# Kernel optimization log

Hardware: AMD Instinct MI355X
Metric: run time of the kernel (lower is better)

## Reference

```python
import jax, jax.numpy as jnp
import numpy as np

N_NODES = 50000
NUM_FEATS = 512
HIDDEN = 128
NUM_LAYERS = 4
NUM_CLASSES = 40
N_EDGES = 800000
ALPHA = 0.1
C_MIN = 0.2
RESIDUAL_WEIGHT = C_MIN - ALPHA  # 0.1
BIAS_SRELU = -10.0


def setup_inputs() -> dict:
    key = jax.random.key(0)
    ks = jax.random.split(key, 8)
    x = jax.random.normal(ks[0], (N_NODES, NUM_FEATS), dtype=jnp.float32)
    edge_index = jax.random.randint(ks[1], (2, N_EDGES), 0, N_NODES, dtype=jnp.int64)
    W_in = jax.random.normal(ks[2], (NUM_FEATS, HIDDEN), dtype=jnp.float32) / np.sqrt(NUM_FEATS)
    b_in = jnp.zeros((HIDDEN,), dtype=jnp.float32)
    W_layers = jax.random.normal(ks[3], (NUM_LAYERS, HIDDEN, HIDDEN), dtype=jnp.float32) / np.sqrt(HIDDEN)
    srelu_bias = jnp.full((NUM_LAYERS, HIDDEN), BIAS_SRELU, dtype=jnp.float32)
    W_out = jax.random.normal(ks[4], (HIDDEN, NUM_CLASSES), dtype=jnp.float32) / np.sqrt(HIDDEN)
    b_out = jnp.zeros((NUM_CLASSES,), dtype=jnp.float32)
    return {"x": x, "edge_index": edge_index, "W_in": W_in, "b_in": b_in,
            "W_layers": W_layers, "srelu_bias": srelu_bias,
            "W_out": W_out, "b_out": b_out}


def _gcn_norm(edge_index, n):
    # PyG gcn_norm: add self-loops, symmetric normalization D^-1/2 A D^-1/2
    loop = jnp.arange(n, dtype=edge_index.dtype)
    src = jnp.concatenate([edge_index[0], loop])
    dst = jnp.concatenate([edge_index[1], loop])
    ones = jnp.ones(src.shape[0], dtype=jnp.float32)
    deg = jax.ops.segment_sum(ones, dst, num_segments=n)
    dinv = jnp.where(deg > 0, jax.lax.rsqrt(deg), 0.0)
    norm = dinv[src] * dinv[dst]  # [E+N]
    return src, dst, norm


def reference(x, edge_index, W_in, b_in, W_layers, srelu_bias, W_out, b_out):
    n = x.shape[0]
    src, dst, norm = _gcn_norm(edge_index, n)

    # input layer (eval mode: dropout is identity), non-arxiv path
    h = jax.nn.relu(x @ W_in + b_in)
    x0 = h  # original_x residual anchor

    def layer(h, params):
        W, sb = params
        # sparse gather-scale-scatter aggregation: [E, H] messages
        agg = jax.ops.segment_sum(norm[:, None] * h[src], dst, num_segments=n)
        out = (1.0 - ALPHA - RESIDUAL_WEIGHT) * agg + RESIDUAL_WEIGHT * h + ALPHA * x0
        out = out @ W
        out = jax.nn.relu(out - sb) + sb  # SReLU
        return out, None

    h, _ = jax.lax.scan(layer, h, (W_layers, srelu_bias))
    return h @ W_out + b_out
```

## Files before the change

kernel.cpp:

```cpp
#include <hip/hip_runtime.h>
#include <hip/hip_fp16.h>

#define N_NODES 50000
#define E_EDGES 800000
#define F_IN 512
#define HID 128
#define N_LAYERS 4
#define C_OUT 40
#define SCAN_BLOCKS 196

typedef __attribute__((ext_vector_type(8))) short bf16x8;
typedef __attribute__((ext_vector_type(4))) float f32x4;

#define MFMA16(a, b, c) __builtin_amdgcn_mfma_f32_16x16x32_bf16(a, b, c, 0, 0, 0)

__device__ __forceinline__ void split2(float a, unsigned short& hi, unsigned short& lo) {
    unsigned u = __float_as_uint(a);
    unsigned r = u + 0x7FFFu + ((u >> 16) & 1u);
    hi = (unsigned short)(r >> 16);
    float hf = __uint_as_float(((unsigned)hi) << 16);
    lo = (unsigned short)(__float_as_uint(a - hf) >> 16);
}

__device__ __forceinline__ void async16(void* lds, const void* g) {
    __builtin_amdgcn_global_load_lds(
        (const __attribute__((address_space(1))) unsigned*)g,
        (__attribute__((address_space(3))) unsigned*)lds, 16, 0, 0);
}

__global__ void indeg_count(const int* __restrict__ ei, int* __restrict__ indeg) {
    int e = blockIdx.x * 256 + threadIdx.x;
    if (e < E_EDGES) {
        unsigned d = (unsigned)ei[E_EDGES + e];
        if (d < N_NODES) atomicAdd(&indeg[d], 1);
    }
}

__global__ void scan_p1(const int* __restrict__ indeg, int* __restrict__ bsum,
                        float* __restrict__ dinv) {
    __shared__ int red[4];
    int i = blockIdx.x * 256 + threadIdx.x;
    int v = (i < N_NODES) ? indeg[i] : 0;
    if (i < N_NODES) dinv[i] = rsqrtf(1.0f + (float)v);
    int s = v;
    #pragma unroll
    for (int off = 32; off > 0; off >>= 1) s += __shfl_down(s, off, 64);
    if ((threadIdx.x & 63) == 0) red[threadIdx.x >> 6] = s;
    __syncthreads();
    if (threadIdx.x == 0) bsum[blockIdx.x] = red[0] + red[1] + red[2] + red[3];
}

__launch_bounds__(256)
__global__ void scan_p2(const int* __restrict__ bsum, int* __restrict__ boff,
                        int* __restrict__ rowptr) {
    __shared__ int s[256];
    int t = threadIdx.x;
    int v = (t < SCAN_BLOCKS) ? bsum[t] : 0;
    s[t] = v;
    __syncthreads();
    #pragma unroll
    for (int off = 1; off < 256; off <<= 1) {
        int a = s[t];
        int b = (t >= off) ? s[t - off] : 0;
        __syncthreads();
        s[t] = a + b;
        __syncthreads();
    }
    if (t < SCAN_BLOCKS) boff[t] = (t == 0) ? 0 : s[t - 1];
    if (t == 255) rowptr[N_NODES] = s[SCAN_BLOCKS - 1];
}

__launch_bounds__(256)
__global__ void scan_p3(const int* __restrict__ indeg, const int* __restrict__ boff,
                        int* __restrict__ rowptr, int* __restrict__ cursor) {
    __shared__ int s[256];
    int t = threadIdx.x;
    int i = blockIdx.x * 256 + t;
    int v = (i < N_NODES) ? indeg[i] : 0;
    s[t] = v;
    __syncthreads();
    #pragma unroll
    for (int off = 1; off < 256; off <<= 1) {
        int a = s[t];
        int b = (t >= off) ? s[t - off] : 0;
        __syncthreads();
        s[t] = a + b;
        __syncthreads();
    }
    if (i < N_NODES) {
        int excl = boff[blockIdx.x] + s[t] - v;
        rowptr[i] = excl;
        cursor[i] = excl;
    }
}

__global__ void csr_fill(const int* __restrict__ ei, int* __restrict__ cursor,
                         int* __restrict__ csr) {
    int e = blockIdx.x * 256 + threadIdx.x;
    if (e < E_EDGES) {
        unsigned s = (unsigned)ei[e];
        unsigned d = (unsigned)ei[E_EDGES + e];
        if (s < N_NODES && d < N_NODES) {
            int pos = atomicAdd(&cursor[d], 1);
            csr[pos] = (int)s;
        }
    }
}

__global__ void wprep(const float* __restrict__ Wi, const float* __restrict__ Wl,
                      const float* __restrict__ Wo,
                      unsigned short* __restrict__ Wth, unsigned short* __restrict__ Wtl,
                      unsigned short* __restrict__ Wlth, unsigned short* __restrict__ Wltl,
                      unsigned short* __restrict__ Woth, unsigned short* __restrict__ Wotl) {
    int idx = blockIdx.x * 256 + threadIdx.x;
    unsigned short hi, lo;
    if (idx < F_IN * HID) {
        int k = idx >> 7, n = idx & 127;
        split2(Wi[idx], hi, lo);
        Wth[(size_t)n * F_IN + k] = hi;
        Wtl[(size_t)n * F_IN + k] = lo;
    } else if (idx < 2 * F_IN * HID) {
        int j = idx - F_IN * HID;
        int l = j >> 14, rem = j & 16383;
        int k = rem >> 7, n = rem & 127;
        split2(Wl[j], hi, lo);
        Wlth[(size_t)l * HID * HID + n * HID + k] = hi;
        Wltl[(size_t)l * HID * HID + n * HID + k] = lo;
    } else if (idx < 2 * F_IN * HID + 48 * HID) {
        int j = idx - 2 * F_IN * HID;
        int n = j >> 7, k = j & 127;
        float w = (n < C_OUT) ? Wo[(size_t)k * C_OUT + n] : 0.f;
        split2(w, hi, lo);
        Woth[(size_t)n * HID + k] = hi;
        Wotl[(size_t)n * HID + k] = lo;
    }
}

__launch_bounds__(256)
__global__ void gemm_in_mfma(const float* __restrict__ x,
                             const unsigned short* __restrict__ Bth,
                             const unsigned short* __restrict__ Btl,
                             const float* __restrict__ bi,
                             const float* __restrict__ dinv,
                             float* __restrict__ x0out,
                             __half* __restrict__ g16) {
    __shared__ __align__(16) unsigned short Ah[64 * 32];
    __shared__ __align__(16) unsigned short Al[64 * 32];
    __shared__ __align__(16) unsigned short Bh[128 * 32];
    __shared__ __align__(16) unsigned short Bl[128 * 32];
    const int t = threadIdx.x;
    const int lane = t & 63;
    const int wv = t >> 6;
    const int wr = wv >> 1, wc = wv & 1;
    const int row0 = blockIdx.x * 64;
    const int fr = lane & 15;
    const int fkg = lane >> 4;
    const float4 z4 = make_float4(0.f, 0.f, 0.f, 0.f);

    f32x4 acc[2][4] = {};

    auto stageB = [&](int k0) {
        #pragma unroll
        for (int i = 0; i < 2; i++) {
            int g = t + i * 256;
            int n = g >> 2, kg = g & 3;
            int kgp = kg ^ ((n >> 1) & 3);
            size_t src = (size_t)n * F_IN + k0 + kgp * 8;
            async16(&Bh[g * 8], &Bth[src]);
            async16(&Bl[g * 8], &Btl[src]);
        }
    };
    auto loadA = [&](int k0, float4* xr) {
        #pragma unroll
        for (int i = 0; i < 2; i++) {
            int q = t + i * 256;
            int r = q >> 3, c4 = q & 7;
            int grow = row0 + r;
            xr[i] = (grow < N_NODES) ? *(const float4*)&x[(size_t)grow * F_IN + k0 + c4 * 4] : z4;
        }
    };
    auto writeA = [&](const float4* xr) {
        #pragma unroll
        for (int i = 0; i < 2; i++) {
            int q = t + i * 256;
            int r = q >> 3, c4 = q & 7;
            ushort4 uh, ul;
            split2(xr[i].x, uh.x, ul.x); split2(xr[i].y, uh.y, ul.y);
            split2(xr[i].z, uh.z, ul.z); split2(xr[i].w, uh.w, ul.w);
            int gp = (c4 >> 1) ^ ((r >> 1) & 3);
            int idx = r * 32 + gp * 8 + (c4 & 1) * 4;
            *(ushort4*)&Ah[idx] = uh;
            *(ushort4*)&Al[idx] = ul;
        }
    };

    float4 xa[2], xn[2];
    loadA(0, xa);

    for (int step = 0; step < 16; step++) {
        stageB(step * 32);
        writeA(xa);
        if (step < 15) loadA((step + 1) * 32, xn);
        __syncthreads();

        bf16x8 ah[2], al[2];
        #pragma unroll
        for (int mt = 0; mt < 2; mt++) {
            int arow = wr * 32 + mt * 16 + fr;
            int aidx = arow * 32 + (fkg ^ ((arow >> 1) & 3)) * 8;
            ah[mt] = *(bf16x8*)&Ah[aidx];
            al[mt] = *(bf16x8*)&Al[aidx];
        }
        #pragma unroll
        for (int nt = 0; nt < 4; nt++) {
            int n = wc * 64 + nt * 16 + fr;
            int bidx = n * 32 + (fkg ^ ((n >> 1) & 3)) * 8;
            bf16x8 bh = *(bf16x8*)&Bh[bidx];
            bf16x8 bl = *(bf16x8*)&Bl[bidx];
            #pragma unroll
            for (int mt = 0; mt < 2; mt++) {
                acc[mt][nt] = MFMA16(al[mt], bh, acc[mt][nt]);
                acc[mt][nt] = MFMA16(ah[mt], bl, acc[mt][nt]);
                acc[mt][nt] = MFMA16(ah[mt], bh, acc[mt][nt]);
            }
        }
        __syncthreads();
        xa[0] = xn[0]; xa[1] = xn[1];
    }

    const int dcol = lane & 15;
    const int dr0 = (lane >> 4) * 4;
    float dv[2][4];
    #pragma unroll
    for (int mt = 0; mt < 2; mt++)
        #pragma unroll
        for (int j = 0; j < 4; j++) {
            int grow = row0 + wr * 32 + mt * 16 + dr0 + j;
            dv[mt][j] = (grow < N_NODES) ? dinv[grow] : 0.f;
        }
    #pragma unroll
    for (int nt = 0; nt < 4; nt++) {
        int gcol = wc * 64 + nt * 16 + dcol;
        float b = bi[gcol];
        #pragma unroll
        for (int mt = 0; mt < 2; mt++) {
            #pragma unroll
            for (int j = 0; j < 4; j++) {
                int grow = row0 + wr * 32 + mt * 16 + dr0 + j;
                if (grow < N_NODES) {
                    float v = fmaxf(acc[mt][nt][j] + b, 0.f);
                    x0out[(size_t)grow * HID + gcol] = v;
                    g16[(size_t)grow * HID + gcol] = __float2half(dv[mt][j] * v);
                }
            }
        }
    }
}

__launch_bounds__(256)
__global__ void aggregate(const int* __restrict__ rowptr, const int* __restrict__ csr,
                          const float* __restrict__ dinv,
                          const __half* __restrict__ g16,
                          const float* __restrict__ h, const float* __restrict__ x0,
                          float* __restrict__ comb) {
    const int node = blockIdx.x * 4 + (threadIdx.x >> 6);
    const int lane = threadIdx.x & 63;
    if (node >= N_NODES) return;

    const unsigned* g32 = (const unsigned*)g16;
    const float dd = dinv[node];
    const int beg = rowptr[node];
    const int end = rowptr[node + 1];

    float a0 = 0.f, a1 = 0.f, b0 = 0.f, b1 = 0.f;

    #define GACC(r, i) { \
        __half2 p = *(__half2*)&(r); \
        float2 f = __half22float2(p); \
        if ((i) & 1) { b0 += f.x; b1 += f.y; } else { a0 += f.x; a1 += f.y; } }

    int e = beg;
    for (; e + 16 <= end; e += 16) {
        unsigned r[16];
        #pragma unroll
        for (int i = 0; i < 16; i++) r[i] = g32[(size_t)csr[e + i] * 64 + lane];
        #pragma unroll
        for (int i = 0; i < 16; i++) GACC(r[i], i)
    }
    for (; e + 4 <= end; e += 4) {
        unsigned r[4];
        #pragma unroll
        for (int i = 0; i < 4; i++) r[i] = g32[(size_t)csr[e + i] * 64 + lane];
        #pragma unroll
        for (int i = 0; i < 4; i++) GACC(r[i], i)
    }
    for (; e < end; e++) {
        unsigned r = g32[(size_t)csr[e] * 64 + lane];
        GACC(r, 0)
    }
    #undef GACC

    float s0 = a0 + b0, s1 = a1 + b1;
    const float c1 = 0.8f * dd;
    const float c2 = 0.8f * dd * dd + 0.1f;
    float2 hv = ((const float2*)h)[(size_t)node * 64 + lane];
    float2 xv = ((const float2*)x0)[(size_t)node * 64 + lane];
    float2 o;
    o.x = fmaf(c1, s0, fmaf(c2, hv.x, 0.1f * xv.x));
    o.y = fmaf(c1, s1, fmaf(c2, hv.y, 0.1f * xv.y));
    ((float2*)comb)[(size_t)node * 64 + lane] = o;
}

__launch_bounds__(256)
__global__ void gemm_layer_mfma(const unsigned short* __restrict__ Bth,
                                const unsigned short* __restrict__ Btl,
                                const float* __restrict__ sb,
                                const float* __restrict__ dinv,
                                float* __restrict__ comb,
                                __half* __restrict__ g16) {
    __shared__ __align__(16) unsigned short Ah[64 * 128];
    __shared__ __align__(16) unsigned short Al[64 * 128];
    __shared__ __align__(16) unsigned short Bh[128 * 32];
    __shared__ __align__(16) unsigned short Bl[128 * 32];
    const int t = threadIdx.x;
    const int lane = t & 63;
    const int wv = t >> 6;
    const int wr = wv >> 1, wc = wv & 1;
    const int row0 = blockIdx.x * 64;
    const int fr = lane & 15;
    const int fkg = lane >> 4;

    f32x4 acc[2][4] = {};

    auto stageB = [&](int k0) {
        #pragma unroll
        for (int i = 0; i < 2; i++) {
            int g = t + i * 256;
            int n = g >> 2, kg = g & 3;
            int kgp = kg ^ ((n >> 1) & 3);
            size_t src = (size_t)n * HID + k0 + kgp * 8;
            async16(&Bh[g * 8], &Bth[src]);
            async16(&Bl[g * 8], &Btl[src]);
        }
    };

    stageB(0);
    #pragma unroll
    for (int i = 0; i < 8; i++) {
        int q = t + i * 256;
        int r = q >> 5, c4 = q & 31;
        int grow = row0 + r;
        float4 v = make_float4(0.f, 0.f, 0.f, 0.f);
        if (grow < N_NODES) v = *(const float4*)&comb[(size_t)grow * HID + c4 * 4];
        ushort4 uh, ul;
        split2(v.x, uh.x, ul.x); split2(v.y, uh.y, ul.y);
        split2(v.z, uh.z, ul.z); split2(v.w, uh.w, ul.w);
        int idx = (r * 128 + c4 * 4) ^ ((r & 7) << 3);
        *(ushort4*)&Ah[idx] = uh;
        *(ushort4*)&Al[idx] = ul;
    }
    __syncthreads();

    #pragma unroll
    for (int step = 0; step < 4; step++) {
        bf16x8 ah[2], al[2];
        #pragma unroll
        for (int mt = 0; mt < 2; mt++) {
            int arow = wr * 32 + mt * 16 + fr;
            int aidx = (arow * 128 + step * 32 + fkg * 8) ^ ((arow & 7) << 3);
            ah[mt] = *(bf16x8*)&Ah[aidx];
            al[mt] = *(bf16x8*)&Al[aidx];
        }
        #pragma unroll
        for (int nt = 0; nt < 4; nt++) {
            int n = wc * 64 + nt * 16 + fr;
            int bidx = n * 32 + (fkg ^ ((n >> 1) & 3)) * 8;
            bf16x8 bh = *(bf16x8*)&Bh[bidx];
            bf16x8 bl = *(bf16x8*)&Bl[bidx];
            #pragma unroll
            for (int mt = 0; mt < 2; mt++) {
                acc[mt][nt] = MFMA16(al[mt], bh, acc[mt][nt]);
                acc[mt][nt] = MFMA16(ah[mt], bl, acc[mt][nt]);
                acc[mt][nt] = MFMA16(ah[mt], bh, acc[mt][nt]);
            }
        }
        __syncthreads();
        if (step < 3) {
            stageB((step + 1) * 32);
            __syncthreads();
        }
    }

    const int dcol = lane & 15;
    const int dr0 = (lane >> 4) * 4;
    float dv[2][4];
    #pragma unroll
    for (int mt = 0; mt < 2; mt++)
        #pragma unroll
        for (int j = 0; j < 4; j++) {
            int grow = row0 + wr * 32 + mt * 16 + dr0 + j;
            dv[mt][j] = (grow < N_NODES) ? dinv[grow] : 0.f;
        }
    #pragma unroll
    for (int nt = 0; nt < 4; nt++) {
        int gcol = wc * 64 + nt * 16 + dcol;
        float s = sb[gcol];
        #pragma unroll
        for (int mt = 0; mt < 2; mt++) {
            #pragma unroll
            for (int j = 0; j < 4; j++) {
                int grow = row0 + wr * 32 + mt * 16 + dr0 + j;
                if (grow < N_NODES) {
                    float v = fmaxf(acc[mt][nt][j], s);
                    comb[(size_t)grow * HID + gcol] = v;
                    g16[(size_t)grow * HID + gcol] = __float2half(dv[mt][j] * v);
                }
            }
        }
    }
}

__launch_bounds__(256)
__global__ void gemm_layer_out(const unsigned short* __restrict__ Bth,
                               const unsigned short* __restrict__ Btl,
                               const float* __restrict__ sb,
                               const unsigned short* __restrict__ Woth,
                               const unsigned short* __restrict__ Wotl,
                               const float* __restrict__ bo,
                               const float* __restrict__ comb,
                               float* __restrict__ out) {
    __shared__ __align__(16) unsigned short Ah[64 * 128];
    __shared__ __align__(16) unsigned short Al[64 * 128];
    __shared__ __align__(16) unsigned short Bh[128 * 32];
    __shared__ __align__(16) unsigned short Bl[128 * 32];
    const int t = threadIdx.x;
    const int lane = t & 63;
    const int wv = t >> 6;
    const int wr = wv >> 1, wc = wv & 1;
    const int row0 = blockIdx.x * 64;
    const int fr = lane & 15;
    const int fkg = lane >> 4;

    f32x4 acc[2][4] = {};

    auto stageB = [&](int k0) {
        #pragma unroll
        for (int i = 0; i < 2; i++) {
            int g = t + i * 256;
            int n = g >> 2, kg = g & 3;
            int kgp = kg ^ ((n >> 1) & 3);
            size_t src = (size_t)n * HID + k0 + kgp * 8;
            async16(&Bh[g * 8], &Bth[src]);
            async16(&Bl[g * 8], &Btl[src]);
        }
    };

    stageB(0);
    #pragma unroll
    for (int i = 0; i < 8; i++) {
        int q = t + i * 256;
        int r = q >> 5, c4 = q & 31;
        int grow = row0 + r;
        float4 v = make_float4(0.f, 0.f, 0.f, 0.f);
        if (grow < N_NODES) v = *(const float4*)&comb[(size_t)grow * HID + c4 * 4];
        ushort4 uh, ul;
        split2(v.x, uh.x, ul.x); split2(v.y, uh.y, ul.y);
        split2(v.z, uh.z, ul.z); split2(v.w, uh.w, ul.w);
        int idx = (r * 128 + c4 * 4) ^ ((r & 7) << 3);
        *(ushort4*)&Ah[idx] = uh;
        *(ushort4*)&Al[idx] = ul;
    }
    __syncthreads();

    #pragma unroll
    for (int step = 0; step < 4; step++) {
        bf16x8 ah[2], al[2];
        #pragma unroll
        for (int mt = 0; mt < 2; mt++) {
            int arow = wr * 32 + mt * 16 + fr;
            int aidx = (arow * 128 + step * 32 + fkg * 8) ^ ((arow & 7) << 3);
            ah[mt] = *(bf16x8*)&Ah[aidx];
            al[mt] = *(bf16x8*)&Al[aidx];
        }
        #pragma unroll
        for (int nt = 0; nt < 4; nt++) {
            int n = wc * 64 + nt * 16 + fr;
            int bidx = n * 32 + (fkg ^ ((n >> 1) & 3)) * 8;
            bf16x8 bh = *(bf16x8*)&Bh[bidx];
            bf16x8 bl = *(bf16x8*)&Bl[bidx];
            #pragma unroll
            for (int mt = 0; mt < 2; mt++) {
                acc[mt][nt] = MFMA16(al[mt], bh, acc[mt][nt]);
                acc[mt][nt] = MFMA16(ah[mt], bl, acc[mt][nt]);
                acc[mt][nt] = MFMA16(ah[mt], bh, acc[mt][nt]);
            }
        }
        __syncthreads();
        if (step < 3) {
            stageB((step + 1) * 32);
            __syncthreads();
        }
    }

    const int dcol = lane & 15;
    const int dr0 = (lane >> 4) * 4;
    #pragma unroll
    for (int nt = 0; nt < 4; nt++) {
        int col = wc * 64 + nt * 16 + dcol;
        float s = sb[col];
        #pragma unroll
        for (int mt = 0; mt < 2; mt++) {
            #pragma unroll
            for (int j = 0; j < 4; j++) {
                int row = wr * 32 + mt * 16 + dr0 + j;
                float v = fmaxf(acc[mt][nt][j], s);
                unsigned short hi, lo;
                split2(v, hi, lo);
                int idx = (row * 128 + col) ^ ((row & 7) << 3);
                Ah[idx] = hi;
                Al[idx] = lo;
            }
        }
    }
    __syncthreads();

    f32x4 oacc[3] = {};
    #pragma unroll
    for (int kk = 0; kk < 4; kk++) {
        int arow = wv * 16 + fr;
        int aidx = (arow * 128 + kk * 32 + fkg * 8) ^ ((arow & 7) << 3);
        bf16x8 ah = *(bf16x8*)&Ah[aidx];
        bf16x8 al = *(bf16x8*)&Al[aidx];
        #pragma unroll
        for (int nt = 0; nt < 3; nt++) {
            size_t boff = (size_t)(nt * 16 + fr) * HID + kk * 32 + fkg * 8;
            bf16x8 bh = *(const bf16x8*)&Woth[boff];
            bf16x8 bl = *(const bf16x8*)&Wotl[boff];
            oacc[nt] = MFMA16(al, bh, oacc[nt]);
            oacc[nt] = MFMA16(ah, bl, oacc[nt]);
            oacc[nt] = MFMA16(ah, bh, oacc[nt]);
        }
    }
    #pragma unroll
    for (int nt = 0; nt < 3; nt++) {
        int gcol = nt * 16 + dcol;
        if (gcol < C_OUT) {
            float b = bo[gcol];
            #pragma unroll
            for (int j = 0; j < 4; j++) {
                int grow = row0 + wv * 16 + dr0 + j;
                if (grow < N_NODES)
                    out[(size_t)grow * C_OUT + gcol] = oacc[nt][j] + b;
            }
        }
    }
}

extern "C" void kernel_launch(void* const* d_in, const int* in_sizes, int n_in,
                              void* d_out, int out_size, void* d_ws, size_t ws_size,
                              hipStream_t stream) {
    const float* x   = (const float*)d_in[0];
    const int*   ei  = (const int*)d_in[1];
    const float* Wi  = (const float*)d_in[2];
    const float* bi  = (const float*)d_in[3];
    const float* Wls = (const float*)d_in[4];
    const float* sbs = (const float*)d_in[5];
    const float* Wo  = (const float*)d_in[6];
    const float* bo  = (const float*)d_in[7];
    float* out = (float*)d_out;

    float* dinv    = (float*)d_ws;
    int*   indeg   = (int*)(dinv + 50176);
    int*   rowptr  = indeg + 50176;
    int*   cursor  = rowptr + 50304;
    int*   bsum    = cursor + 50176;
    int*   boff    = bsum + 256;
    int*   csr     = boff + 256;
    unsigned short* Wth  = (unsigned short*)(csr + 800000);
    unsigned short* Wtl  = Wth + 65536;
    unsigned short* Wlth = Wtl + 65536;
    unsigned short* Wltl = Wlth + 65536;
    unsigned short* Woth = Wltl + 65536;
    unsigned short* Wotl = Woth + 6144;
    float* x0  = (float*)(Wotl + 6144);
    float* hB  = x0 + (size_t)N_NODES * HID;
    float* hC  = hB + (size_t)N_NODES * HID;
    __half* g16 = (__half*)(hC + (size_t)N_NODES * HID);

    const int edgeBlocks = (E_EDGES + 255) / 256;
    const int gemmBlocks = (N_NODES + 63) / 64;
    const int aggBlocks  = (N_NODES + 3) / 4;
    const int wprepBlocks = (2 * F_IN * HID + 48 * HID + 255) / 256;

    hipMemsetAsync(indeg, 0, N_NODES * sizeof(int), stream);
    indeg_count<<<edgeBlocks, 256, 0, stream>>>(ei, indeg);
    scan_p1<<<SCAN_BLOCKS, 256, 0, stream>>>(indeg, bsum, dinv);
    scan_p2<<<1, 256, 0, stream>>>(bsum, boff, rowptr);
    scan_p3<<<SCAN_BLOCKS, 256, 0, stream>>>(indeg, boff, rowptr, cursor);
    csr_fill<<<edgeBlocks, 256, 0, stream>>>(ei, cursor, csr);
    wprep<<<wprepBlocks, 256, 0, stream>>>(Wi, Wls, Wo, Wth, Wtl, Wlth, Wltl, Woth, Wotl);

    gemm_in_mfma<<<gemmBlocks, 256, 0, stream>>>(x, Wth, Wtl, bi, dinv, x0, g16);

    float* h = x0;
    for (int l = 0; l < N_LAYERS - 1; l++) {
        float* next = (l & 1) ? hC : hB;
        aggregate<<<aggBlocks, 256, 0, stream>>>(rowptr, csr, dinv, g16, h, x0, next);
        gemm_layer_mfma<<<gemmBlocks, 256, 0, stream>>>(Wlth + (size_t)l * HID * HID,
                                                        Wltl + (size_t)l * HID * HID,
                                                        sbs + (size_t)l * HID, dinv,
                                                        next, g16);
        h = next;
    }
    aggregate<<<aggBlocks, 256, 0, stream>>>(rowptr, csr, dinv, g16, h, x0, hC);
    gemm_layer_out<<<gemmBlocks, 256, 0, stream>>>(Wlth + (size_t)3 * HID * HID,
                                                   Wltl + (size_t)3 * HID * HID,
                                                   sbs + (size_t)3 * HID,
                                                   Woth, Wotl, bo, hC, out);
}
```

Baseline: 403.7 us.

## Slice fp16 feature buffer into column blocks for cache-local aggregation

Stores the fp16 scaled-feature buffer as eight column slices of 16 halves per node. The aggregate kernel now assigns each block one slice, so every gathered row fetch is a 32-byte segment and the working set per slice is about 1.6 MB, which can stay cache-resident during the random neighbour gathers. Each wave now handles 8 nodes with 8 lanes each. The input GEMM also drops its register prefetch of the next A tile, which simplifies the code but exposes global load latency. The trade-off is that the csr index list is re-read once per slice, and gathers are narrower per lane.

```diff
diff --git a/kernel.cpp b/kernel.cpp
--- a/kernel.cpp
+++ b/kernel.cpp
@@ -13,6 +13,8 @@
 typedef __attribute__((ext_vector_type(4))) float f32x4;
 
 #define MFMA16(a, b, c) __builtin_amdgcn_mfma_f32_16x16x32_bf16(a, b, c, 0, 0, 0)
+
+#define G16OFF(node, col) ((size_t)((col) >> 4) * (N_NODES * 16) + (size_t)(node) * 16 + ((col) & 15))
 
 __device__ __forceinline__ void split2(float a, unsigned short& hi, unsigned short& lo) {
     unsigned u = __float_as_uint(a);
@@ -155,11 +157,11 @@
     const int row0 = blockIdx.x * 64;
     const int fr = lane & 15;
     const int fkg = lane >> 4;
-    const float4 z4 = make_float4(0.f, 0.f, 0.f, 0.f);
 
     f32x4 acc[2][4] = {};
 
-    auto stageB = [&](int k0) {
+    for (int step = 0; step < 16; step++) {
+        const int k0 = step * 32;
         #pragma unroll
         for (int i = 0; i < 2; i++) {
             int g = t + i * 256;
@@ -169,38 +171,21 @@
             async16(&Bh[g * 8], &Bth[src]);
             async16(&Bl[g * 8], &Btl[src]);
         }
-    };
-    auto loadA = [&](int k0, float4* xr) {
         #pragma unroll
         for (int i = 0; i < 2; i++) {
             int q = t + i * 256;
             int r = q >> 3, c4 = q & 7;
             int grow = row0 + r;
-            xr[i] = (grow < N_NODES) ? *(const float4*)&x[(size_t)grow * F_IN + k0 + c4 * 4] : z4;
-        }
-    };
-    auto writeA = [&](const float4* xr) {
-        #pragma unroll
-        for (int i = 0; i < 2; i++) {
-            int q = t + i * 256;
-            int r = q >> 3, c4 = q & 7;
+            float4 v = make_float4(0.f, 0.f, 0.f, 0.f);
+            if (grow < N_NODES) v = *(const float4*)&x[(size_t)grow * F_IN + k0 + c4 * 4];
             ushort4 uh, ul;
-            split2(xr[i].x, uh.x, ul.x); split2(xr[i].y, uh.y, ul.y);
-            split2(xr[i].z, uh.z, ul.z); split2(xr[i].w, uh.w, ul.w);
+            split2(v.x, uh.x, ul.x); split2(v.y, uh.y, ul.y);
+            split2(v.z, uh.z, ul.z); split2(v.w, uh.w, ul.w);
             int gp = (c4 >> 1) ^ ((r >> 1) & 3);
             int idx = r * 32 + gp * 8 + (c4 & 1) * 4;
             *(ushort4*)&Ah[idx] = uh;
             *(ushort4*)&Al[idx] = ul;
         }
-    };
-
-    float4 xa[2], xn[2];
-    loadA(0, xa);
-
-    for (int step = 0; step < 16; step++) {
-        stageB(step * 32);
-        writeA(xa);
-        if (step < 15) loadA((step + 1) * 32, xn);
         __syncthreads();
 
         bf16x8 ah[2], al[2];
@@ -225,7 +210,6 @@
             }
         }
         __syncthreads();
-        xa[0] = xn[0]; xa[1] = xn[1];
     }
 
     const int dcol = lane & 15;
@@ -250,7 +234,7 @@
                 if (grow < N_NODES) {
                     float v = fmaxf(acc[mt][nt][j] + b, 0.f);
                     x0out[(size_t)grow * HID + gcol] = v;
-                    g16[(size_t)grow * HID + gcol] = __float2half(dv[mt][j] * v);
+                    g16[G16OFF(grow, gcol)] = __float2half(dv[mt][j] * v);
                 }
             }
         }
@@ -263,52 +247,70 @@
                           const __half* __restrict__ g16,
                           const float* __restrict__ h, const float* __restrict__ x0,
                           float* __restrict__ comb) {
-    const int node = blockIdx.x * 4 + (threadIdx.x >> 6);
+    const int slice = blockIdx.x & 7;
+    const int chunk = blockIdx.x >> 3;
     const int lane = threadIdx.x & 63;
+    const int wv = threadIdx.x >> 6;
+    const int ng = lane >> 3;
+    const int dw = lane & 7;
+    const int node = chunk * 32 + wv * 8 + ng;
     if (node >= N_NODES) return;
 
-    const unsigned* g32 = (const unsigned*)g16;
-    const float dd = dinv[node];
+    const unsigned* gs = (const unsigned*)g16 + (size_t)slice * (N_NODES * 8);
     const int beg = rowptr[node];
     const int end = rowptr[node + 1];
 
     float a0 = 0.f, a1 = 0.f, b0 = 0.f, b1 = 0.f;
 
-    #define GACC(r, i) { \
-        __half2 p = *(__half2*)&(r); \
-        float2 f = __half22float2(p); \
-        if ((i) & 1) { b0 += f.x; b1 += f.y; } else { a0 += f.x; a1 += f.y; } }
-
     int e = beg;
-    for (; e + 16 <= end; e += 16) {
-        unsigned r[16];
-        #pragma unroll
-        for (int i = 0; i < 16; i++) r[i] = g32[(size_t)csr[e + i] * 64 + lane];
-        #pragma unroll
-        for (int i = 0; i < 16; i++) GACC(r[i], i)
-    }
-    for (; e + 4 <= end; e += 4) {
-        unsigned r[4];
-        #pragma unroll
-        for (int i = 0; i < 4; i++) r[i] = g32[(size_t)csr[e + i] * 64 + lane];
-        #pragma unroll
-        for (int i = 0; i < 4; i++) GACC(r[i], i)
-    }
-    for (; e < end; e++) {
-        unsigned r = g32[(size_t)csr[e] * 64 + lane];
-        GACC(r, 0)
-    }
-    #undef GACC
-
-    float s0 = a0 + b0, s1 = a1 + b1;
+    for (; e + 8 <= end; e += 8) {
+        int s0 = csr[e + 0], s1 = csr[e + 1], s2 = csr[e + 2], s3 = csr[e + 3];
+        int s4 = csr[e + 4], s5 = csr[e + 5], s6 = csr[e + 6], s7 = csr[e + 7];
+        unsigned r0 = gs[(size_t)s0 * 8 + dw];
+        unsigned r1 = gs[(size_t)s1 * 8 + dw];
+        unsigned r2 = gs[(size_t)s2 * 8 + dw];
+        unsigned r3 = gs[(size_t)s3 * 8 + dw];
+        unsigned r4 = gs[(size_t)s4 * 8 + dw];
+        unsigned r5 = gs[(size_t)s5 * 8 + dw];
+        unsigned r6 = gs[(size_t)s6 * 8 + dw];
+        unsigned r7 = gs[(size_t)s7 * 8 + dw];
+        float2 f0 = __half22float2(*(__half2*)&r0);
+        float2 f1 = __half22float2(*(__half2*)&r1);
+        float2 f2 = __half22float2(*(__half2*)&r2);
+        float2 f3 = __half22float2(*(__half2*)&r3);
+        float2 f4 = __half22float2(*(__half2*)&r4);
+        float2 f5 = __half22float2(*(__half2*)&r5);
+        float2 f6 = __half22float2(*(__half2*)&r6);
+        float2 f7 = __half22float2(*(__half2*)&r7);
+        a0 += f0.x; a1 += f0.y; b0 += f1.x; b1 += f1.y;
+        a0 += f2.x; a1 += f2.y; b0 += f3.x; b1 += f3.y;
+        a0 += f4.x; a1 += f4.y; b0 += f5.x; b1 += f5.y;
+        a0 += f6.x; a1 += f6.y; b0 += f7.x; b1 += f7.y;
+    }
+    for (; e + 2 <= end; e += 2) {
+        int s0 = csr[e], s1 = csr[e + 1];
+        unsigned r0 = gs[(size_t)s0 * 8 + dw];
+        unsigned r1 = gs[(size_t)s1 * 8 + dw];
+        float2 f0 = __half22float2(*(__half2*)&r0);
+        float2 f1 = __half22float2(*(__half2*)&r1);
+        a0 += f0.x; a1 += f0.y; b0 += f1.x; b1 += f1.y;
+    }
+    if (e < end) {
+        unsigned r = gs[(size_t)csr[e] * 8 + dw];
+        float2 f = __half22float2(*(__half2*)&r);
+        a0 += f.x; a1 += f.y;
+    }
+
+    float s0f = a0 + b0, s1f = a1 + b1;
+    const float dd = dinv[node];
     const float c1 = 0.8f * dd;
     const float c2 = 0.8f * dd * dd + 0.1f;
-    float2 hv = ((const float2*)h)[(size_t)node * 64 + lane];
-    float2 xv = ((const float2*)x0)[(size_t)node * 64 + lane];
+    float2 hv = ((const float2*)h)[(size_t)node * 64 + slice * 8 + dw];
+    float2 xv = ((const float2*)x0)[(size_t)node * 64 + slice * 8 + dw];
     float2 o;
-    o.x = fmaf(c1, s0, fmaf(c2, hv.x, 0.1f * xv.x));
-    o.y = fmaf(c1, s1, fmaf(c2, hv.y, 0.1f * xv.y));
-    ((float2*)comb)[(size_t)node * 64 + lane] = o;
+    o.x = fmaf(c1, s0f, fmaf(c2, hv.x, 0.1f * xv.x));
+    o.y = fmaf(c1, s1f, fmaf(c2, hv.y, 0.1f * xv.y));
+    ((float2*)comb)[(size_t)node * 64 + slice * 8 + dw] = o;
 }
 
 __launch_bounds__(256)
@@ -413,7 +415,7 @@
                 if (grow < N_NODES) {
                     float v = fmaxf(acc[mt][nt][j], s);
                     comb[(size_t)grow * HID + gcol] = v;
-                    g16[(size_t)grow * HID + gcol] = __float2half(dv[mt][j] * v);
+                    g16[G16OFF(grow, gcol)] = __float2half(dv[mt][j] * v);
                 }
             }
         }
@@ -589,7 +591,7 @@
 
     const int edgeBlocks = (E_EDGES + 255) / 256;
     const int gemmBlocks = (N_NODES + 63) / 64;
-    const int aggBlocks  = (N_NODES + 3) / 4;
+    const int aggBlocks  = 8 * ((N_NODES + 31) / 32);
     const int wprepBlocks = (2 * F_IN * HID + 48 * HID + 255) / 256;
 
     hipMemsetAsync(indeg, 0, N_NODES * sizeof(int), stream);
```

After: 428.4 us. +6.1%, slower.
